# Performance work log

Hardware: AMD Instinct MI355X
Metric: run time of the kernel (lower is better)

Reference implementation:

```python
import jax, jax.numpy as jnp
import numpy as np

RANK, A1, A2, B1, B2, BATCH = 16, 64, 8, 64, 8, 32768

def setup_inputs() -> dict:
    key = jax.random.key(0)
    kx, ks, ka, kb, kbias = jax.random.split(key, 5)
    # Params drawn as small gaussians (stand-in for xavier init; exact init
    x = jax.random.normal(kx, (BATCH, A1 * B1), dtype=jnp.float32)
    s = jax.random.normal(ks, (A1, A2), dtype=jnp.float32)
    a = jax.random.normal(ka, (RANK, A1, A2), dtype=jnp.float32) * 0.05
    b = jax.random.normal(kb, (RANK, B1, B2), dtype=jnp.float32) * 0.05
    bias = jax.random.normal(kbias, (A2 * B2,), dtype=jnp.float32)
    return {"x": x, "s": s, "a": a, "b": b, "bias": bias}

def reference(x, s, a, b, bias):
    # sa[r] = s * a[r]   (elementwise scale shared across ranks)
    sa = s[None, :, :] * a                                    # (r, a1, a2)
    # w = sum_r kron(sa[r], b[r]): w[i*b1+k, j*b2+l] = sum_r sa[r,i,j] b[r,k,l]
    # w is only (a1*b1, a2*b2) = (4096, 64), cheap to materialize here.
    w = jnp.einsum('rij,rkl->ikjl', sa, b).reshape(A1 * B1, A2 * B2)
    return x @ w + bias[None, :]                              # (batch, a2*b2)
```

## Files before the change

### kernel.cpp

```cpp
#include <hip/hip_runtime.h>
#include <hip/hip_bf16.h>

#define RANK 16
#define BATCH 32768
#define K_DIM 4096
#define N_DIM 64
#define CHUNK 128
#define NCHUNK 32
#define ROWB 64

typedef __bf16 bf16x8 __attribute__((ext_vector_type(8)));
typedef float floatx4 __attribute__((ext_vector_type(4)));
typedef unsigned short ushort8 __attribute__((ext_vector_type(8)));

#define WAITVM(n) asm volatile("s_waitcnt vmcnt(" #n ")" ::: "memory")
#define BARRIER() asm volatile("s_barrier" ::: "memory")

__device__ inline unsigned short f2bf(float f) {
  unsigned u = __builtin_bit_cast(unsigned, f);
  u += 0x7fffu + ((u >> 16) & 1u);
  return (unsigned short)(u >> 16);
}

__device__ inline bf16x8 cvt8(float4 a0, float4 a1) {
  ushort8 au;
  au[0] = f2bf(a0.x); au[1] = f2bf(a0.y); au[2] = f2bf(a0.z); au[3] = f2bf(a0.w);
  au[4] = f2bf(a1.x); au[5] = f2bf(a1.y); au[6] = f2bf(a1.z); au[7] = f2bf(a1.w);
  return __builtin_bit_cast(bf16x8, au);
}

__global__ __launch_bounds__(256) void build_wF(
    const float* __restrict__ s, const float* __restrict__ a,
    const float* __restrict__ b, unsigned short* __restrict__ wF) {
  int e = blockIdx.x * 256 + threadIdx.x;
  int j    = e & 7;
  int lane = (e >> 3) & 63;
  int ks   = (e >> 9) & 127;
  int cg   = e >> 16;
  int n = cg * 16 + (lane & 15);
  int k = ks * 32 + ((lane >> 4) << 3) + j;
  int i = k >> 6, kk = k & 63, jj = n >> 3, ll = n & 7;
  float acc = 0.f;
  #pragma unroll
  for (int r = 0; r < RANK; ++r) {
    acc += a[r * 512 + i * 8 + jj] * b[r * 512 + kk * 8 + ll];
  }
  acc *= s[i * 8 + jj];
  wF[e] = f2bf(acc);
}

__global__ __launch_bounds__(256, 2) void kron_gemm(
    const float* __restrict__ x, const unsigned short* __restrict__ wF,
    const float* __restrict__ bias, float* __restrict__ out) {
  __shared__ __align__(16) float As[2][ROWB * CHUNK];

  const int tid  = threadIdx.x;
  const int lane = tid & 63;
  const int wave = tid >> 6;
  const int ln15 = lane & 15;
  const int kseg = lane >> 4;
  const int m0   = blockIdx.x * ROWB;
  const int rhalf = lane >> 5;

  floatx4 acc[4] = {};

  struct W4 { bf16x8 t[4]; };

  auto loadw = [&](int c) {
    W4 w;
    #pragma unroll
    for (int t = 0; t < 4; ++t)
      w.t[t] = *(const bf16x8*)(wF + (((size_t)(wave * 128 + c * 4 + t)) << 9)
                                + (lane << 3));
    return w;
  };

  auto stage = [&](float* buf, int c) {
    #pragma unroll
    for (int p = 0; p < 8; ++p) {
      const int rbase = wave * 16 + 2 * p;
      const int row   = rbase + rhalf;
      const int sb    = ((lane & 31) << 4) ^ ((row & 7) << 4);
      const float* src = x + (size_t)(m0 + row) * K_DIM + c * CHUNK + (sb >> 2);
      float* dst = buf + rbase * CHUNK;
      __builtin_amdgcn_global_load_lds(
          (const __attribute__((address_space(1))) void*)(const void*)src,
          (__attribute__((address_space(3))) void*)(void*)dst, 16, 0, 0);
    }
  };

  auto compute = [&](const float* buf, const W4& w) {
    const char* Ab = (const char*)buf;
    #pragma unroll
    for (int t = 0; t < 4; ++t) {
      #pragma unroll
      for (int f = 0; f < 4; ++f) {
        const int row = f * 16 + ln15;
        const int swz = (row & 7) << 4;
        const int b0  = t * 128 + kseg * 32;
        float4 lo = *(const float4*)(Ab + row * 512 + ((b0)      ^ swz));
        float4 hi = *(const float4*)(Ab + row * 512 + ((b0 + 16) ^ swz));
        acc[f] = __builtin_amdgcn_mfma_f32_16x16x32_bf16(cvt8(lo, hi), w.t[t],
                                                         acc[f], 0, 0, 0);
      }
    }
  };

  float* A0 = &As[0][0];
  float* A1 = &As[1][0];

  W4 wA = loadw(0);
  stage(A0, 0);

  #pragma unroll 1
  for (int i = 0; i < 15; ++i) {
    const int c = 2 * i;
    W4 wB = loadw(c + 1);
    stage(A1, c + 1);
    WAITVM(12);
    BARRIER();
    compute(A0, wA);
    BARRIER();

    wA = loadw(c + 2);
    stage(A0, c + 2);
    WAITVM(12);
    BARRIER();
    compute(A1, wB);
    BARRIER();
  }
  {
    W4 wB = loadw(31);
    stage(A1, 31);
    WAITVM(12);
    BARRIER();
    compute(A0, wA);
    BARRIER();
    WAITVM(0);
    BARRIER();
    compute(A1, wB);
  }

  const int col = wave * 16 + ln15;
  const float bv = bias[col];
  #pragma unroll
  for (int f = 0; f < 4; ++f) {
    float* op = out + (size_t)(m0 + f * 16 + kseg * 4) * N_DIM + col;
    #pragma unroll
    for (int r = 0; r < 4; ++r)
      op[(size_t)r * N_DIM] = acc[f][r] + bv;
  }
}

extern "C" void kernel_launch(void* const* d_in, const int* in_sizes, int n_in,
                              void* d_out, int out_size, void* d_ws, size_t ws_size,
                              hipStream_t stream) {
  const float* x    = (const float*)d_in[0];
  const float* s    = (const float*)d_in[1];
  const float* a    = (const float*)d_in[2];
  const float* b    = (const float*)d_in[3];
  const float* bias = (const float*)d_in[4];
  float* out = (float*)d_out;
  unsigned short* wF = (unsigned short*)d_ws;

  build_wF<<<1024, 256, 0, stream>>>(s, a, b, wF);
  kron_gemm<<<BATCH / ROWB, 256, 0, stream>>>(x, wF, bias, out);
}
```

Measured before the change: 121.1 us.

## Use 512-thread 128-row blocks with shared LDS weight staging and coalesced output

Doubles rows per block to 128 with 8 waves split into column groups and row halves, so each weight tile is staged once into LDS via global_load_lds and shared by two waves instead of every wave loading it into registers. The K chunk is halved to 64 to fit the LDS budget, and the swizzle is changed to match the new row width. Output is staged through LDS and written as coalesced float4 stores. In exchange there are twice as many barrier-synchronised iterations, occupancy drops to one block per CU, and there are fewer blocks overall.

```diff
diff --git a/kernel.cpp b/kernel.cpp
--- a/kernel.cpp
+++ b/kernel.cpp
@@ -5,9 +5,9 @@
 #define BATCH 32768
 #define K_DIM 4096
 #define N_DIM 64
-#define CHUNK 128
-#define NCHUNK 32
-#define ROWB 64
+#define CHUNK 64
+#define NCHUNK 64
+#define ROWB 128
 
 typedef __bf16 bf16x8 __attribute__((ext_vector_type(8)));
 typedef float floatx4 __attribute__((ext_vector_type(4)));
@@ -49,106 +49,108 @@
   wF[e] = f2bf(acc);
 }
 
-__global__ __launch_bounds__(256, 2) void kron_gemm(
+__global__ __launch_bounds__(512, 1) void kron_gemm(
     const float* __restrict__ x, const unsigned short* __restrict__ wF,
     const float* __restrict__ bias, float* __restrict__ out) {
-  __shared__ __align__(16) float As[2][ROWB * CHUNK];
+  __shared__ __align__(16) float          As[2][ROWB * CHUNK];
+  __shared__ __align__(16) unsigned short Ws[2][8][512];
 
   const int tid  = threadIdx.x;
   const int lane = tid & 63;
   const int wave = tid >> 6;
+  const int cg   = wave & 3;
+  const int rh   = wave >> 2;
   const int ln15 = lane & 15;
   const int kseg = lane >> 4;
   const int m0   = blockIdx.x * ROWB;
-  const int rhalf = lane >> 5;
 
   floatx4 acc[4] = {};
 
-  struct W4 { bf16x8 t[4]; };
-
-  auto loadw = [&](int c) {
-    W4 w;
+  auto stage = [&](int buf, int c) {
     #pragma unroll
-    for (int t = 0; t < 4; ++t)
-      w.t[t] = *(const bf16x8*)(wF + (((size_t)(wave * 128 + c * 4 + t)) << 9)
-                                + (lane << 3));
-    return w;
-  };
-
-  auto stage = [&](float* buf, int c) {
-    #pragma unroll
-    for (int p = 0; p < 8; ++p) {
-      const int rbase = wave * 16 + 2 * p;
-      const int row   = rbase + rhalf;
-      const int sb    = ((lane & 31) << 4) ^ ((row & 7) << 4);
+    for (int p = 0; p < 4; ++p) {
+      const int rbase = wave * 16 + 4 * p;
+      const int row   = rbase + (lane >> 4);
+      const int sb    = ((lane & 15) << 4) ^ ((row & 15) << 4);
       const float* src = x + (size_t)(m0 + row) * K_DIM + c * CHUNK + (sb >> 2);
-      float* dst = buf + rbase * CHUNK;
+      float* dst = &As[buf][rbase * CHUNK];
+      __builtin_amdgcn_global_load_lds(
+          (const __attribute__((address_space(1))) void*)(const void*)src,
+          (__attribute__((address_space(3))) void*)(void*)dst, 16, 0, 0);
+    }
+    {
+      const int scg = wave >> 1, st = wave & 1;
+      const unsigned short* src =
+          wF + (((size_t)(scg * 128 + c * 2 + st)) << 9) + (lane << 3);
+      unsigned short* dst = &Ws[buf][scg * 2 + st][0];
       __builtin_amdgcn_global_load_lds(
           (const __attribute__((address_space(1))) void*)(const void*)src,
           (__attribute__((address_space(3))) void*)(void*)dst, 16, 0, 0);
     }
   };
 
-  auto compute = [&](const float* buf, const W4& w) {
-    const char* Ab = (const char*)buf;
+  auto compute = [&](int buf) {
+    const char* Ab = (const char*)&As[buf][0];
     #pragma unroll
-    for (int t = 0; t < 4; ++t) {
+    for (int t = 0; t < 2; ++t) {
+      bf16x8 wf = *(const bf16x8*)&Ws[buf][cg * 2 + t][lane << 3];
       #pragma unroll
       for (int f = 0; f < 4; ++f) {
-        const int row = f * 16 + ln15;
-        const int swz = (row & 7) << 4;
+        const int row = rh * 64 + f * 16 + ln15;
+        const int swz = (row & 15) << 4;
         const int b0  = t * 128 + kseg * 32;
-        float4 lo = *(const float4*)(Ab + row * 512 + ((b0)      ^ swz));
-        float4 hi = *(const float4*)(Ab + row * 512 + ((b0 + 16) ^ swz));
-        acc[f] = __builtin_amdgcn_mfma_f32_16x16x32_bf16(cvt8(lo, hi), w.t[t],
+        float4 lo = *(const float4*)(Ab + row * 256 + ((b0)      ^ swz));
+        float4 hi = *(const float4*)(Ab + row * 256 + ((b0 + 16) ^ swz));
+        acc[f] = __builtin_amdgcn_mfma_f32_16x16x32_bf16(cvt8(lo, hi), wf,
                                                          acc[f], 0, 0, 0);
       }
     }
   };
 
-  float* A0 = &As[0][0];
-  float* A1 = &As[1][0];
-
-  W4 wA = loadw(0);
-  stage(A0, 0);
+  stage(0, 0);
 
   #pragma unroll 1
-  for (int i = 0; i < 15; ++i) {
+  for (int i = 0; i < NCHUNK / 2 - 1; ++i) {
     const int c = 2 * i;
-    W4 wB = loadw(c + 1);
-    stage(A1, c + 1);
-    WAITVM(12);
+    stage(1, c + 1);
+    WAITVM(5);
     BARRIER();
-    compute(A0, wA);
+    compute(0);
     BARRIER();
 
-    wA = loadw(c + 2);
-    stage(A0, c + 2);
-    WAITVM(12);
+    stage(0, c + 2);
+    WAITVM(5);
     BARRIER();
-    compute(A1, wB);
+    compute(1);
     BARRIER();
   }
   {
-    W4 wB = loadw(31);
-    stage(A1, 31);
-    WAITVM(12);
+    stage(1, NCHUNK - 1);
+    WAITVM(5);
     BARRIER();
-    compute(A0, wA);
+    compute(0);
     BARRIER();
     WAITVM(0);
     BARRIER();
-    compute(A1, wB);
+    compute(1);
   }
 
-  const int col = wave * 16 + ln15;
+  float* A0 = &As[0][0];
+  const int col = cg * 16 + ln15;
   const float bv = bias[col];
   #pragma unroll
   for (int f = 0; f < 4; ++f) {
-    float* op = out + (size_t)(m0 + f * 16 + kseg * 4) * N_DIM + col;
     #pragma unroll
     for (int r = 0; r < 4; ++r)
-      op[(size_t)r * N_DIM] = acc[f][r] + bv;
+      A0[(rh * 64 + f * 16 + kseg * 4 + r) * N_DIM + col] = acc[f][r] + bv;
+  }
+  __syncthreads();
+  float4* og = (float4*)(out + (size_t)m0 * N_DIM);
+  const float4* ol = (const float4*)A0;
+  #pragma unroll
+  for (int p = 0; p < 4; ++p) {
+    const int fi = p * 512 + tid;
+    og[fi] = ol[fi];
   }
 }
 
@@ -164,5 +166,5 @@
   unsigned short* wF = (unsigned short*)d_ws;
 
   build_wF<<<1024, 256, 0, stream>>>(s, a, b, wF);
-  kron_gemm<<<BATCH / ROWB, 256, 0, stream>>>(x, wF, bias, out);
+  kron_gemm<<<BATCH / ROWB, 512, 0, stream>>>(x, wF, bias, out);
 }
```

New measurement: 154.3 us. 1.27x slower.
